# Kernel tuning notes

Measured on AMD Instinct MI355X. Metric: run time of the kernel, lower is better.

## Reference

```python
import jax, jax.numpy as jnp
import numpy as np

H = 1024      # hidden_size
NH = 16       # num_heads
HD = H // NH  # head_dim
FF = 4 * H    # ffn hidden


def setup_inputs() -> dict:
    key = jax.random.key(0)
    ks = jax.random.split(key, 11)
    s = 1.0 / np.sqrt(H)
    inp = {
        "x": jax.random.normal(ks[0], (2, 2048, H), dtype=jnp.float32),
        "Wq": jax.random.uniform(ks[1], (H, H), jnp.float32, -s, s),
        "Wk": jax.random.uniform(ks[2], (H, H), jnp.float32, -s, s),
        "Wv": jax.random.uniform(ks[3], (H, H), jnp.float32, -s, s),
        "Wo": jax.random.uniform(ks[4], (H, H), jnp.float32, -s, s),
        "ln1_g": jnp.ones((H,), jnp.float32),
        "ln1_b": jnp.zeros((H,), jnp.float32),
        "ln2_g": jnp.ones((H,), jnp.float32),
        "ln2_b": jnp.zeros((H,), jnp.float32),
        "W1": jax.random.uniform(ks[5], (H, FF), jnp.float32, -s, s),
        "b1": jnp.zeros((FF,), jnp.float32),
        "W2": jax.random.uniform(ks[6], (FF, H), jnp.float32, -1.0 / np.sqrt(FF), 1.0 / np.sqrt(FF)),
        "b2": jnp.zeros((H,), jnp.float32),
    }
    return inp


def _layernorm(x, g, b, eps=1e-5):
    mu = jnp.mean(x, axis=-1, keepdims=True)
    var = jnp.mean(jnp.square(x - mu), axis=-1, keepdims=True)
    return (x - mu) * jax.lax.rsqrt(var + eps) * g + b


def reference(x, Wq, Wk, Wv, Wo, ln1_g, ln1_b, ln2_g, ln2_b, W1, b1, W2, b2):
    bsz, seq, _ = x.shape
    h = _layernorm(x, ln1_g, ln1_b)
    # project and split heads: [b, s, H] -> [b, nh, s, hd]
    def split(t):
        return t.reshape(bsz, seq, NH, HD).transpose(0, 2, 1, 3)
    q = split(h @ Wq.T)
    k = split(h @ Wk.T)
    v = split(h @ Wv.T)
    scores = jnp.einsum("bhqd,bhkd->bhqk", q, k) / jnp.sqrt(jnp.float32(HD))
    probs = jax.nn.softmax(scores, axis=-1)
    attn = jnp.einsum("bhqk,bhkd->bhqd", probs, v)
    attn = attn.transpose(0, 2, 1, 3).reshape(bsz, seq, H)
    x = x + attn @ Wo.T
    h2 = _layernorm(x, ln2_g, ln2_b)
    ffn = jax.nn.gelu(h2 @ W1 + b1, approximate=False) @ W2 + b2
    return x + ffn
```

## Files before the change

### kernel.cpp

```cpp
#include <hip/hip_runtime.h>
#include <stdint.h>
#include <math.h>

typedef float f32x4 __attribute__((ext_vector_type(4)));
typedef __bf16 bf16x8 __attribute__((ext_vector_type(8)));

#define DEVI __device__ __forceinline__

#if __has_builtin(__builtin_amdgcn_exp2f)
#define EXP2(x) __builtin_amdgcn_exp2f(x)
#else
#define EXP2(x) exp2f(x)
#endif

#define LOG2E 1.44269504f

DEVI unsigned short f2bf(float f) {
  union { float f; unsigned int u; } c; c.f = f;
  unsigned int u = c.u;
  return (unsigned short)((u + 0x7FFFu + ((u >> 16) & 1u)) >> 16);
}

DEVI unsigned short f2bf_fast(float f) {
  union { float f; unsigned int u; } c; c.f = f;
  return (unsigned short)((c.u + 0x8000u) >> 16);
}

DEVI void gll16(const void* g, void* l) {
  __builtin_amdgcn_global_load_lds(
      (const __attribute__((address_space(1))) void*)g,
      (__attribute__((address_space(3))) void*)l,
      16, 0, 0);
}

__global__ __launch_bounds__(256) void f32_to_bf16_k(
    const float* __restrict__ in, unsigned short* __restrict__ out, int n4) {
  int i = blockIdx.x * 256 + threadIdx.x;
  if (i >= n4) return;
  float4 v = ((const float4*)in)[i];
  ushort4 ov;
  ov.x = f2bf(v.x); ov.y = f2bf(v.y); ov.z = f2bf(v.z); ov.w = f2bf(v.w);
  ((ushort4*)out)[i] = ov;
}

__global__ __launch_bounds__(256) void transpose_f32_bf16(
    const float* __restrict__ in, unsigned short* __restrict__ out, int R, int C) {
  __shared__ float tile[32][33];
  int bc = blockIdx.x * 32, br = blockIdx.y * 32;
  int tx = threadIdx.x & 31, ty = threadIdx.x >> 5;
#pragma unroll
  for (int i = 0; i < 32; i += 8)
    tile[ty + i][tx] = in[(size_t)(br + ty + i) * C + bc + tx];
  __syncthreads();
#pragma unroll
  for (int i = 0; i < 32; i += 8)
    out[(size_t)(bc + ty + i) * R + br + tx] = f2bf(tile[tx][ty + i]);
}

__global__ __launch_bounds__(256) void vtrans(
    const unsigned short* __restrict__ QKV, unsigned short* __restrict__ Vt) {
  int stile = blockIdx.x;
  int bh = blockIdx.y;
  int b = bh >> 4, h = bh & 15;
  __shared__ unsigned short tile[64][68];
  const unsigned short* src =
      QKV + ((size_t)(b * 2048 + stile * 64)) * 3072 + 2048 + h * 64;
  int t = threadIdx.x;
#pragma unroll
  for (int i = 0; i < 16; i++) {
    int e = i * 256 + t; int s = e >> 6, d = e & 63;
    tile[s][d] = src[(size_t)s * 3072 + d];
  }
  __syncthreads();
  unsigned short* dst = Vt + (size_t)bh * 64 * 2048 + stile * 64;
#pragma unroll
  for (int i = 0; i < 16; i++) {
    int e = i * 256 + t; int d = e >> 6, s = e & 63;
    dst[(size_t)d * 2048 + s] = tile[s][d];
  }
}

__global__ __launch_bounds__(256) void layernorm_bf16(
    const float* __restrict__ x, const float* __restrict__ g,
    const float* __restrict__ be, unsigned short* __restrict__ out) {
  const int row = blockIdx.x;
  const int t = threadIdx.x;
  const float4 v = ((const float4*)(x + (size_t)row * 1024))[t];
  float s = v.x + v.y + v.z + v.w;
  float s2 = v.x * v.x + v.y * v.y + v.z * v.z + v.w * v.w;
#pragma unroll
  for (int d = 32; d > 0; d >>= 1) {
    s += __shfl_down(s, d);
    s2 += __shfl_down(s2, d);
  }
  __shared__ float ps[4], ps2[4], st[2];
  const int lane = t & 63, wave = t >> 6;
  if (lane == 0) { ps[wave] = s; ps2[wave] = s2; }
  __syncthreads();
  if (t == 0) {
    float S = ps[0] + ps[1] + ps[2] + ps[3];
    float S2 = ps2[0] + ps2[1] + ps2[2] + ps2[3];
    float mu = S * (1.0f / 1024.0f);
    float var = S2 * (1.0f / 1024.0f) - mu * mu;
    st[0] = mu; st[1] = rsqrtf(var + 1e-5f);
  }
  __syncthreads();
  float mu = st[0], inv = st[1];
  float4 gv = ((const float4*)g)[t];
  float4 bv = ((const float4*)be)[t];
  ushort4 ov;
  ov.x = f2bf((v.x - mu) * inv * gv.x + bv.x);
  ov.y = f2bf((v.y - mu) * inv * gv.y + bv.y);
  ov.z = f2bf((v.z - mu) * inv * gv.z + bv.z);
  ov.w = f2bf((v.w - mu) * inv * gv.w + bv.w);
  ((ushort4*)(out + (size_t)row * 1024))[t] = ov;
}

DEVI float gelu_f(float x) {
  float a = x * (2.3022082f + 0.1029432f * x * x);
  return x / (1.0f + EXP2(-a));
}

template <int EPI, int TM, int TN>
__global__ __launch_bounds__(256) void gemm_bt(
    const unsigned short* __restrict__ A, const unsigned short* __restrict__ B,
    int M, int N, int K, float* __restrict__ outF, unsigned short* __restrict__ outB,
    const float* __restrict__ res, const float* __restrict__ bias) {
  __shared__ __align__(16) unsigned short As[2][TM * 32];
  __shared__ __align__(16) unsigned short Bs[2][TN * 32];
  constexpr int MF = TM / 32;
  constexpr int NF = TN / 32;
  const int t = threadIdx.x;
  const int lane = t & 63, wave = t >> 6;
  const int wr = wave >> 1, wc = wave & 1;
  const int l15 = lane & 15, lg = lane >> 4;
  const int sl = (t & 7) ^ ((t >> 3) & 7);
  const int srow2 = ((t >> 3) << 1) + (sl >> 2);
  const int scol2 = (sl & 3) * 8;
  const int gx = gridDim.x;
  const int nwg = gx * gridDim.y;
  const int orig = blockIdx.y * gx + blockIdx.x;
  const int swz = (orig & 7) * (nwg >> 3) + (orig >> 3);
  const int bx = swz % gx, by = swz / gx;
  const size_t aBase = (size_t)by * TM * K;
  const size_t bBase = (size_t)bx * TN * K;
  f32x4 acc[MF][NF] = {};

  auto stage = [&](int buf, int kt) {
#pragma unroll
    for (int i = 0; i < TM / 64; i++)
      gll16(A + aBase + (size_t)(srow2 + i * 64) * K + kt + scol2,
            (char*)&As[buf][0] + i * 4096 + t * 16);
#pragma unroll
    for (int i = 0; i < TN / 64; i++)
      gll16(B + bBase + (size_t)(srow2 + i * 64) * K + kt + scol2,
            (char*)&Bs[buf][0] + i * 4096 + t * 16);
  };

  stage(0, 0);
  __syncthreads();
  const int nk = K >> 5;
  for (int ki = 0; ki < nk; ki++) {
    const int cur = ki & 1;
    if (ki + 1 < nk) stage(cur ^ 1, (ki + 1) << 5);
    bf16x8 af[MF], bfv[NF];
#pragma unroll
    for (int m = 0; m < MF; m++) {
      const int R = wr * (TM / 2) + m * 16 + l15;
      const int r = R >> 1;
      const int ps = (((R & 1) << 2) | lg) ^ (r & 7);
      af[m] = *(const bf16x8*)&As[cur][r * 64 + ps * 8];
    }
#pragma unroll
    for (int n = 0; n < NF; n++) {
      const int R = wc * (TN / 2) + n * 16 + l15;
      const int r = R >> 1;
      const int ps = (((R & 1) << 2) | lg) ^ (r & 7);
      bfv[n] = *(const bf16x8*)&Bs[cur][r * 64 + ps * 8];
    }
#pragma unroll
    for (int m = 0; m < MF; m++)
#pragma unroll
      for (int n = 0; n < NF; n++)
        acc[m][n] = __builtin_amdgcn_mfma_f32_16x16x32_bf16(af[m], bfv[n], acc[m][n], 0, 0, 0);
    __syncthreads();
  }
  const int rowB = by * TM + wr * (TM / 2);
  const int colB = bx * TN + wc * (TN / 2);
#pragma unroll
  for (int m = 0; m < MF; m++) {
#pragma unroll
    for (int n = 0; n < NF; n++) {
#pragma unroll
      for (int r = 0; r < 4; r++) {
        int gm = rowB + m * 16 + lg * 4 + r;
        int gn = colB + n * 16 + l15;
        float c = acc[m][n][r];
        size_t idx = (size_t)gm * N + gn;
        if (EPI == 0) {
          outB[idx] = f2bf(c);
        } else if (EPI == 1) {
          outF[idx] = res[idx] + c;
        } else if (EPI == 2) {
          outB[idx] = f2bf(gelu_f(c + bias[gn]));
        } else {
          outF[idx] = res[idx] + c + bias[gn];
        }
      }
    }
  }
}

__global__ __launch_bounds__(256) void attn_flash(
    const unsigned short* __restrict__ QKV, const unsigned short* __restrict__ Vt,
    unsigned short* __restrict__ attnO) {
  __shared__ __align__(16) unsigned short Ks[2][64 * 64];
  __shared__ __align__(16) unsigned short Vs[2][64 * 64];
  __shared__ __align__(16) unsigned short Ps[64 * 64];
  const int t = threadIdx.x;
  const int lane = t & 63, wave = t >> 6;
  const int l15 = lane & 15, lg = lane >> 4;
  const int bid = blockIdx.x;
  const int swzb = (bid & 7) * 128 + (bid >> 3);
  const int qt = swzb & 31;
  const int bh = swzb >> 5;
  const int b = bh >> 4, h = bh & 15;
  const size_t qkvBase = (size_t)b * 2048 * 3072 + (size_t)h * 64;

  bf16x8 aq[2];
  {
    int qrow = qt * 64 + wave * 16 + l15;
    const unsigned short* qp = QKV + qkvBase + (size_t)qrow * 3072;
#pragma unroll
    for (int kc = 0; kc < 2; kc++) {
      aq[kc] = *(const bf16x8*)(qp + kc * 32 + lg * 8);
#pragma unroll
      for (int j = 0; j < 8; j++)
        aq[kc][j] = (__bf16)((float)aq[kc][j] * 0.125f);
    }
  }
  bf16x8 onesf;
#pragma unroll
  for (int j = 0; j < 8; j++) onesf[j] = (__bf16)1.0f;

  const unsigned short* Kg = QKV + qkvBase + 1024;
  const unsigned short* Vg = Vt + (size_t)bh * 64 * 2048;

  f32x4 o[4] = {};
  f32x4 ol = {};
  const float M2 = 4.0f * LOG2E;

  const int srow = t >> 3;
  const int scb = (t & 7) * 16;
  const int e = (scb ^ ((srow & 7) << 4)) >> 1;

  auto stage = [&](int buf, int kt) {
    gll16(Kg + (size_t)(kt * 64 + srow) * 3072 + e, (char*)&Ks[buf][0] + t * 16);
    gll16(Kg + (size_t)(kt * 64 + srow + 32) * 3072 + e, (char*)&Ks[buf][0] + 4096 + t * 16);
    gll16(Vg + (size_t)srow * 2048 + kt * 64 + e, (char*)&Vs[buf][0] + t * 16);
    gll16(Vg + (size_t)(srow + 32) * 2048 + kt * 64 + e, (char*)&Vs[buf][0] + 4096 + t * 16);
  };

  stage(0, 0);
  __syncthreads();

  for (int kt = 0; kt < 32; kt++) {
    const int cur = kt & 1;
    if (kt < 31) stage(cur ^ 1, kt + 1);

    f32x4 s[4];
#pragma unroll
    for (int n = 0; n < 4; n++) {
      s[n] = (f32x4){0.f, 0.f, 0.f, 0.f};
#pragma unroll
      for (int kc = 0; kc < 2; kc++) {
        int r = n * 16 + l15;
        int cb = (kc * 64 + lg * 16) ^ ((r & 7) << 4);
        bf16x8 bk = *(const bf16x8*)&Ks[cur][r * 64 + (cb >> 1)];
        s[n] = __builtin_amdgcn_mfma_f32_16x16x32_bf16(aq[kc], bk, s[n], 0, 0, 0);
      }
    }

#pragma unroll
    for (int n = 0; n < 4; n++)
#pragma unroll
      for (int r = 0; r < 4; r++) {
        int q = wave * 16 + lg * 4 + r;
        int cb = ((n * 16 + l15) * 2) ^ ((q & 7) << 4);
        float p = EXP2(__builtin_fmaf(s[n][r], LOG2E, -M2));
        Ps[q * 64 + (cb >> 1)] = f2bf_fast(p);
      }

#pragma unroll
    for (int kc = 0; kc < 2; kc++) {
      int qr = wave * 16 + l15;
      int cbp = (kc * 64 + lg * 16) ^ ((qr & 7) << 4);
      bf16x8 pa = *(const bf16x8*)&Ps[qr * 64 + (cbp >> 1)];
      ol = __builtin_amdgcn_mfma_f32_16x16x32_bf16(pa, onesf, ol, 0, 0, 0);
#pragma unroll
      for (int n = 0; n < 4; n++) {
        int dr = n * 16 + l15;
        int cbv = (kc * 64 + lg * 16) ^ ((dr & 7) << 4);
        bf16x8 bv = *(const bf16x8*)&Vs[cur][dr * 64 + (cbv >> 1)];
        o[n] = __builtin_amdgcn_mfma_f32_16x16x32_bf16(pa, bv, o[n], 0, 0, 0);
      }
    }
    __syncthreads();
  }

  const int qrow0 = qt * 64 + wave * 16;
  unsigned short* op = attnO + ((size_t)(b * 2048 + qrow0)) * 1024 + h * 64;
  float inv[4];
#pragma unroll
  for (int r = 0; r < 4; r++) inv[r] = 1.0f / ol[r];
#pragma unroll
  for (int n = 0; n < 4; n++)
#pragma unroll
    for (int r = 0; r < 4; r++) {
      int q = lg * 4 + r;
      op[(size_t)q * 1024 + n * 16 + l15] = f2bf(o[n][r] * inv[r]);
    }
}

extern "C" void kernel_launch(void* const* d_in, const int* in_sizes, int n_in,
                              void* d_out, int out_size, void* d_ws, size_t ws_size,
                              hipStream_t stream) {
  const float* x = (const float*)d_in[0];
  const float* Wq = (const float*)d_in[1];
  const float* Wk = (const float*)d_in[2];
  const float* Wv = (const float*)d_in[3];
  const float* Wo = (const float*)d_in[4];
  const float* ln1g = (const float*)d_in[5];
  const float* ln1b = (const float*)d_in[6];
  const float* ln2g = (const float*)d_in[7];
  const float* ln2b = (const float*)d_in[8];
  const float* W1 = (const float*)d_in[9];
  const float* b1 = (const float*)d_in[10];
  const float* W2 = (const float*)d_in[11];
  const float* b2 = (const float*)d_in[12];
  float* out = (float*)d_out;

  char* ws = (char*)d_ws;
  size_t off = 0;
  auto alloc = [&](size_t bytes) {
    void* p = ws + off;
    off += (bytes + 255) & ~(size_t)255;
    return p;
  };
  unsigned short* WB = (unsigned short*)alloc(3072ull * 1024 * 2);
  unsigned short* WoB = (unsigned short*)alloc(1024ull * 1024 * 2);
  unsigned short* W1t = (unsigned short*)alloc(4096ull * 1024 * 2);
  unsigned short* W2t = (unsigned short*)alloc(1024ull * 4096 * 2);
  unsigned short* hb = (unsigned short*)alloc(4096ull * 1024 * 2);
  unsigned short* QKV = (unsigned short*)alloc(4096ull * 3072 * 2);
  unsigned short* attnb = (unsigned short*)alloc(4096ull * 1024 * 2);
  unsigned short* Vtb = (unsigned short*)alloc(32ull * 64 * 2048 * 2);
  float* x2 = (float*)alloc(4096ull * 1024 * 4);
  unsigned short* ffnb = QKV;
  unsigned short* h2b = hb;

  f32_to_bf16_k<<<1024, 256, 0, stream>>>(Wq, WB, 262144);
  f32_to_bf16_k<<<1024, 256, 0, stream>>>(Wk, WB + 1048576, 262144);
  f32_to_bf16_k<<<1024, 256, 0, stream>>>(Wv, WB + 2097152, 262144);
  f32_to_bf16_k<<<1024, 256, 0, stream>>>(Wo, WoB, 262144);
  transpose_f32_bf16<<<dim3(128, 32), 256, 0, stream>>>(W1, W1t, 1024, 4096);
  transpose_f32_bf16<<<dim3(32, 128), 256, 0, stream>>>(W2, W2t, 4096, 1024);
  layernorm_bf16<<<4096, 256, 0, stream>>>(x, ln1g, ln1b, hb);
  gemm_bt<0, 128, 128><<<dim3(24, 32), 256, 0, stream>>>(hb, WB, 4096, 3072, 1024,
                                                         nullptr, QKV, nullptr, nullptr);
  vtrans<<<dim3(32, 32), 256, 0, stream>>>(QKV, Vtb);
  attn_flash<<<1024, 256, 0, stream>>>(QKV, Vtb, attnb);
  gemm_bt<1, 64, 128><<<dim3(8, 64), 256, 0, stream>>>(attnb, WoB, 4096, 1024, 1024,
                                                       x2, nullptr, x, nullptr);
  layernorm_bf16<<<4096, 256, 0, stream>>>(x2, ln2g, ln2b, h2b);
  gemm_bt<2, 128, 128><<<dim3(32, 32), 256, 0, stream>>>(h2b, W1t, 4096, 4096, 1024,
                                                         nullptr, ffnb, nullptr, b1);
  gemm_bt<3, 64, 128><<<dim3(8, 64), 256, 0, stream>>>(ffnb, W2t, 4096, 1024, 4096,
                                                       out, nullptr, x2, b2);
}
```

Before: 263.8 us.

## Enlarge attention query tile, fuse weight conversions, set GEMM occupancy hint

The attention kernel now uses 512-thread blocks, each covering 128 query rows instead of 64. Every K/V tile staged in shared memory is therefore reused by twice as many queries, and each thread issues half as many staging loads. The four weight-conversion launches are merged into one kernel, which removes launch overhead. The GEMM gets a min-blocks-per-CU launch bound of 4, which may constrain register allocation and cause spills.

```diff
diff --git a/kernel.cpp b/kernel.cpp
--- a/kernel.cpp
+++ b/kernel.cpp
@@ -33,14 +33,19 @@
       16, 0, 0);
 }
 
-__global__ __launch_bounds__(256) void f32_to_bf16_k(
-    const float* __restrict__ in, unsigned short* __restrict__ out, int n4) {
+__global__ __launch_bounds__(256) void cvt_weights(
+    const float* __restrict__ Wq, const float* __restrict__ Wk,
+    const float* __restrict__ Wv, const float* __restrict__ Wo,
+    unsigned short* __restrict__ WB, unsigned short* __restrict__ WoB) {
   int i = blockIdx.x * 256 + threadIdx.x;
-  if (i >= n4) return;
-  float4 v = ((const float4*)in)[i];
+  int seg = i >> 18;
+  int j = i & 262143;
+  const float* src = (seg == 0) ? Wq : (seg == 1) ? Wk : (seg == 2) ? Wv : Wo;
+  unsigned short* dst = (seg < 3) ? WB + (size_t)seg * 1048576 : WoB;
+  float4 v = ((const float4*)src)[j];
   ushort4 ov;
   ov.x = f2bf(v.x); ov.y = f2bf(v.y); ov.z = f2bf(v.z); ov.w = f2bf(v.w);
-  ((ushort4*)out)[i] = ov;
+  ((ushort4*)dst)[j] = ov;
 }
 
 __global__ __launch_bounds__(256) void transpose_f32_bf16(
@@ -122,7 +127,7 @@
 }
 
 template <int EPI, int TM, int TN>
-__global__ __launch_bounds__(256) void gemm_bt(
+__global__ __launch_bounds__(256, 4) void gemm_bt(
     const unsigned short* __restrict__ A, const unsigned short* __restrict__ B,
     int M, int N, int K, float* __restrict__ outF, unsigned short* __restrict__ outB,
     const float* __restrict__ res, const float* __restrict__ bias) {
@@ -211,25 +216,25 @@
   }
 }
 
-__global__ __launch_bounds__(256) void attn_flash(
+__global__ __launch_bounds__(512) void attn_flash(
     const unsigned short* __restrict__ QKV, const unsigned short* __restrict__ Vt,
     unsigned short* __restrict__ attnO) {
   __shared__ __align__(16) unsigned short Ks[2][64 * 64];
   __shared__ __align__(16) unsigned short Vs[2][64 * 64];
-  __shared__ __align__(16) unsigned short Ps[64 * 64];
+  __shared__ __align__(16) unsigned short Ps[128 * 64];
   const int t = threadIdx.x;
   const int lane = t & 63, wave = t >> 6;
   const int l15 = lane & 15, lg = lane >> 4;
   const int bid = blockIdx.x;
-  const int swzb = (bid & 7) * 128 + (bid >> 3);
-  const int qt = swzb & 31;
-  const int bh = swzb >> 5;
+  const int swzb = (bid & 7) * 64 + (bid >> 3);
+  const int qt = swzb & 15;
+  const int bh = swzb >> 4;
   const int b = bh >> 4, h = bh & 15;
   const size_t qkvBase = (size_t)b * 2048 * 3072 + (size_t)h * 64;
 
   bf16x8 aq[2];
   {
-    int qrow = qt * 64 + wave * 16 + l15;
+    int qrow = qt * 128 + wave * 16 + l15;
     const unsigned short* qp = QKV + qkvBase + (size_t)qrow * 3072;
 #pragma unroll
     for (int kc = 0; kc < 2; kc++) {
@@ -256,9 +261,7 @@
 
   auto stage = [&](int buf, int kt) {
     gll16(Kg + (size_t)(kt * 64 + srow) * 3072 + e, (char*)&Ks[buf][0] + t * 16);
-    gll16(Kg + (size_t)(kt * 64 + srow + 32) * 3072 + e, (char*)&Ks[buf][0] + 4096 + t * 16);
     gll16(Vg + (size_t)srow * 2048 + kt * 64 + e, (char*)&Vs[buf][0] + t * 16);
-    gll16(Vg + (size_t)(srow + 32) * 2048 + kt * 64 + e, (char*)&Vs[buf][0] + 4096 + t * 16);
   };
 
   stage(0, 0);
@@ -268,10 +271,9 @@
     const int cur = kt & 1;
     if (kt < 31) stage(cur ^ 1, kt + 1);
 
-    f32x4 s[4];
+    f32x4 s[4] = {};
 #pragma unroll
     for (int n = 0; n < 4; n++) {
-      s[n] = (f32x4){0.f, 0.f, 0.f, 0.f};
 #pragma unroll
       for (int kc = 0; kc < 2; kc++) {
         int r = n * 16 + l15;
@@ -281,11 +283,12 @@
       }
     }
 
+    const int q0 = wave * 16 + lg * 4;
 #pragma unroll
     for (int n = 0; n < 4; n++)
 #pragma unroll
       for (int r = 0; r < 4; r++) {
-        int q = wave * 16 + lg * 4 + r;
+        int q = q0 + r;
         int cb = ((n * 16 + l15) * 2) ^ ((q & 7) << 4);
         float p = EXP2(__builtin_fmaf(s[n][r], LOG2E, -M2));
         Ps[q * 64 + (cb >> 1)] = f2bf_fast(p);
@@ -308,7 +311,7 @@
     __syncthreads();
   }
 
-  const int qrow0 = qt * 64 + wave * 16;
+  const int qrow0 = qt * 128 + wave * 16;
   unsigned short* op = attnO + ((size_t)(b * 2048 + qrow0)) * 1024 + h * 64;
   float inv[4];
 #pragma unroll
@@ -359,17 +362,14 @@
   unsigned short* ffnb = QKV;
   unsigned short* h2b = hb;
 
-  f32_to_bf16_k<<<1024, 256, 0, stream>>>(Wq, WB, 262144);
-  f32_to_bf16_k<<<1024, 256, 0, stream>>>(Wk, WB + 1048576, 262144);
-  f32_to_bf16_k<<<1024, 256, 0, stream>>>(Wv, WB + 2097152, 262144);
-  f32_to_bf16_k<<<1024, 256, 0, stream>>>(Wo, WoB, 262144);
+  cvt_weights<<<4096, 256, 0, stream>>>(Wq, Wk, Wv, Wo, WB, WoB);
   transpose_f32_bf16<<<dim3(128, 32), 256, 0, stream>>>(W1, W1t, 1024, 4096);
   transpose_f32_bf16<<<dim3(32, 128), 256, 0, stream>>>(W2, W2t, 4096, 1024);
   layernorm_bf16<<<4096, 256, 0, stream>>>(x, ln1g, ln1b, hb);
   gemm_bt<0, 128, 128><<<dim3(24, 32), 256, 0, stream>>>(hb, WB, 4096, 3072, 1024,
                                                          nullptr, QKV, nullptr, nullptr);
   vtrans<<<dim3(32, 32), 256, 0, stream>>>(QKV, Vtb);
-  attn_flash<<<1024, 256, 0, stream>>>(QKV, Vtb, attnb);
+  attn_flash<<<512, 512, 0, stream>>>(QKV, Vtb, attnb);
   gemm_bt<1, 64, 128><<<dim3(8, 64), 256, 0, stream>>>(attnb, WoB, 4096, 1024, 1024,
                                                        x2, nullptr, x, nullptr);
   layernorm_bf16<<<4096, 256, 0, stream>>>(x2, ln2g, ln2b, h2b);
```

Result: faster. 246.3 us (-6.6%).
